# Optimization experiments

Hardware: AMD Instinct MI355X
Metric: run time of the kernel (lower is better)

## Reference

```python
import jax, jax.numpy as jnp
import numpy as np

N, E, G = 2000, 8000, 100          # nodes, edges, graphs
F_NODE, F_EDGE, H, FC = 22, 4, 128, 64
EPS = 1e-5                          # BatchNorm eps (eval mode, running stats)


def setup_inputs() -> dict:
    key = jax.random.key(0)
    ks = jax.random.split(key, 24)
    rn = lambda k, s, sc=0.1: jax.random.normal(k, s, jnp.float32) * sc
    inp = {}
    inp["x"] = jax.random.normal(ks[0], (N, F_NODE), jnp.float32)
    inp["edge_index"] = jax.random.randint(ks[1], (2, E), 0, N, jnp.int64)
    inp["edge_attr"] = jax.random.uniform(ks[2], (E, F_EDGE), jnp.float32)
    inp["batch"] = jnp.sort(jax.random.randint(ks[3], (N,), 0, G, jnp.int64))
    # edge networks (Linear + ReLU) producing per-edge weight matrices
    inp["We1"] = rn(ks[4], (F_EDGE, F_NODE * H)); inp["be1"] = jnp.zeros((F_NODE * H,), jnp.float32)
    inp["We2"] = rn(ks[5], (F_EDGE, H * H));      inp["be2"] = jnp.zeros((H * H,), jnp.float32)
    inp["We3"] = rn(ks[6], (F_EDGE, H * H));      inp["be3"] = jnp.zeros((H * H,), jnp.float32)
    # NNConv root weights + biases
    inp["Wr1"] = rn(ks[7], (F_NODE, H)); inp["br1"] = jnp.zeros((H,), jnp.float32)
    inp["Wr2"] = rn(ks[8], (H, H));      inp["br2"] = jnp.zeros((H,), jnp.float32)
    inp["Wr3"] = rn(ks[9], (H, H));      inp["br3"] = jnp.zeros((H,), jnp.float32)
    # BatchNorm (eval): gamma, beta, running_mean, running_var
    for i, k in zip((1, 2, 3), (ks[10], ks[11], ks[12])):
        inp[f"g{i}"] = 1.0 + rn(k, (H,), 0.05)
        inp[f"b{i}"] = jnp.zeros((H,), jnp.float32)
        inp[f"rm{i}"] = jnp.zeros((H,), jnp.float32)
        inp[f"rv{i}"] = jnp.ones((H,), jnp.float32)
    # head MLP
    inp["Wf1"] = rn(ks[13], (H, FC)); inp["bf1"] = jnp.zeros((FC,), jnp.float32)
    inp["Wf2"] = rn(ks[14], (FC, 1)); inp["bf2"] = jnp.zeros((1,), jnp.float32)
    return inp


def _nnconv(x, src, dst, edge_attr, We, be, Wr, br, din, dout):
    # per-edge weight matrix from edge features: [E, din, dout]
    w = jax.nn.relu(edge_attr @ We + be).reshape(-1, din, dout)
    msg = jnp.einsum('ei,eio->eo', x[src], w)          # gather + batched matvec
    agg = jax.ops.segment_sum(msg, dst, num_segments=N)  # scatter-add at targets
    return agg + x @ Wr + br                            # root transform + bias


def _bn(x, g, b, rm, rv):
    return (x - rm) * jax.lax.rsqrt(rv + EPS) * g + b


def reference(x, edge_index, edge_attr, batch,
              We1, be1, We2, be2, We3, be3,
              Wr1, br1, Wr2, br2, Wr3, br3,
              g1, b1, rm1, rv1, g2, b2, rm2, rv2, g3, b3, rm3, rv3,
              Wf1, bf1, Wf2, bf2):
    src, dst = edge_index[0], edge_index[1]
    h = jax.nn.relu(_bn(_nnconv(x, src, dst, edge_attr, We1, be1, Wr1, br1, F_NODE, H), g1, b1, rm1, rv1))
    h = jax.nn.relu(_bn(_nnconv(h, src, dst, edge_attr, We2, be2, Wr2, br2, H, H), g2, b2, rm2, rv2))
    h = jax.nn.relu(_bn(_nnconv(h, src, dst, edge_attr, We3, be3, Wr3, br3, H, H), g3, b3, rm3, rv3))
    # global mean pool over graphs
    sums = jax.ops.segment_sum(h, batch, num_segments=G)
    cnts = jax.ops.segment_sum(jnp.ones((N,), h.dtype), batch, num_segments=G)
    pooled = sums / jnp.maximum(cnts, 1.0)[:, None]
    # head MLP (dropout is identity at inference)
    out = jax.nn.relu(pooled @ Wf1 + bf1) @ Wf2 + bf2
    return out  # [G, 1]
```

## Files before the change

### kernel.cpp

```cpp
#include <hip/hip_runtime.h>
#include <hip/hip_bf16.h>
#include <math.h>

#define N_NODES 2000
#define N_EDGES 8000
#define N_GRAPH 100
#define F_NODE 22
#define F_EDGE 4
#define H 128
#define FC 64
#define EPSBN 1e-5f
#define EPB 16
#define EPT 8

#define C1  (F_NODE * H)
#define C1P (24 * H)
#define C2  (H * H)

__global__ __launch_bounds__(256) void precompute_kernel(
    const float* __restrict__ We1, const float* __restrict__ be1,
    const float* __restrict__ We2, const float* __restrict__ We3,
    const float* __restrict__ g1, const float* __restrict__ b1,
    const float* __restrict__ rm1, const float* __restrict__ rv1,
    const float* __restrict__ g2, const float* __restrict__ b2,
    const float* __restrict__ rm2, const float* __restrict__ rv2,
    const float* __restrict__ g3, const float* __restrict__ b3,
    const float* __restrict__ rm3, const float* __restrict__ rv3,
    float4* __restrict__ We1p, float* __restrict__ be1p,
    float4* __restrict__ We2p, float4* __restrict__ We3p,
    float* __restrict__ AB,
    float* __restrict__ sums, float* __restrict__ cnt)
{
    const int t = blockIdx.x * 256 + threadIdx.x;
    const int T1 = C1P, T2 = C1P + C2, T3 = C1P + 2 * C2, T4 = T3 + 3 * H;
    const int T5 = T4 + N_GRAPH * H + N_GRAPH;
    if (t < T1) {
        int j = t;
        if (j < C1) {
            We1p[j] = make_float4(We1[j], We1[C1 + j], We1[2 * C1 + j], We1[3 * C1 + j]);
            be1p[j] = be1[j];
        } else {
            We1p[j] = make_float4(0.f, 0.f, 0.f, 0.f);
            be1p[j] = 0.f;
        }
    } else if (t < T2) {
        int j = t - T1;
        We2p[j] = make_float4(We2[j], We2[C2 + j], We2[2 * C2 + j], We2[3 * C2 + j]);
    } else if (t < T3) {
        int j = t - T2;
        We3p[j] = make_float4(We3[j], We3[C2 + j], We3[2 * C2 + j], We3[3 * C2 + j]);
    } else if (t < T4) {
        int idx = t - T3;
        int l = idx / H, o = idx - l * H;
        const float *g, *b, *rm, *rv;
        if (l == 0) { g = g1; b = b1; rm = rm1; rv = rv1; }
        else if (l == 1) { g = g2; b = b2; rm = rm2; rv = rv2; }
        else { g = g3; b = b3; rm = rm3; rv = rv3; }
        float A = g[o] * rsqrtf(rv[o] + EPSBN);
        AB[l * 2 * H + o] = A;
        AB[l * 2 * H + H + o] = b[o] - rm[o] * A;
    } else if (t < T5) {
        int idx = t - T4;
        if (idx < N_GRAPH * H) sums[idx] = 0.f; else cnt[idx - N_GRAPH * H] = 0.f;
    }
}

template <int DIN, bool ACT>
__global__ __launch_bounds__(256) void root_kernel(
    const float* __restrict__ hin,
    const float* __restrict__ Wr,
    const float* __restrict__ br,
    const float* __restrict__ AB,
    float* __restrict__ outp)
{
    __shared__ float hs[2][DIN];
    const int n0 = blockIdx.x * 2;
    const int tid = threadIdx.x;
    for (int idx = tid; idx < 2 * DIN; idx += 256) {
        int nl = idx / DIN, i = idx - nl * DIN;
        float v = hin[(n0 + nl) * DIN + i];
        if (ACT) v = fmaxf(fmaf(v, AB[i], AB[H + i]), 0.f);
        hs[nl][i] = v;
    }
    __syncthreads();
    const int o = tid & 127;
    const int nl = tid >> 7;
    float acc = br[o];
#pragma unroll 4
    for (int i = 0; i < DIN; i++) acc = fmaf(hs[nl][i], Wr[i * H + o], acc);
    outp[(n0 + nl) * H + o] = acc;
}

template <int DIN, int ISPLIT, int UNR, bool ACT>
__global__ __launch_bounds__(256) void msg_kernel(
    const float* __restrict__ xin,
    const int* __restrict__ ei,
    const float* __restrict__ ea,
    const float4* __restrict__ Wp,
    const float* __restrict__ be,
    const float* __restrict__ AB,
    float* __restrict__ agg)
{
    constexpr int ILEN0 = DIN / ISPLIT;
    constexpr int ILEN = ((ILEN0 + UNR - 1) / UNR) * UNR;
    __shared__ float xs[EPB][ILEN];
    __shared__ float eas[EPB][4];
    __shared__ int dsts[EPB];

    const int nEB = N_EDGES / EPB;
    const int eb = blockIdx.x % nEB;
    const int I0 = (blockIdx.x / nEB) * ILEN0;
    const int e0 = eb * EPB;
    const int tid = threadIdx.x;

    if (tid < EPB * 4) {
        int e = tid >> 2, k = tid & 3;
        eas[e][k] = ea[(e0 + e) * 4 + k];
    }
    if (tid >= 64 && tid < 64 + EPB) {
        dsts[tid - 64] = ei[N_EDGES + e0 + (tid - 64)];
    }
    for (int idx = tid; idx < EPB * ILEN; idx += 256) {
        int e = idx / ILEN, ii = idx - e * ILEN;
        float v = 0.f;
        if (ii < ILEN0) {
            int s = ei[e0 + e];
            v = xin[s * DIN + I0 + ii];
            if (ACT) v = fmaxf(fmaf(v, AB[I0 + ii], AB[H + I0 + ii]), 0.f);
        }
        xs[e][ii] = v;
    }
    __syncthreads();

    const int o = tid & 127;
    const int eh = tid >> 7;

    float acc[EPT];
    float ear[EPT][4];
#pragma unroll
    for (int q = 0; q < EPT; q++) {
        acc[q] = 0.f;
#pragma unroll
        for (int k = 0; k < 4; k++) ear[q][k] = eas[eh * EPT + q][k];
    }

#pragma unroll 1
    for (int ii = 0; ii < ILEN; ii += UNR) {
        float4 w4[UNR];
        float bb[UNR];
#pragma unroll
        for (int u = 0; u < UNR; u++) {
            w4[u] = Wp[(I0 + ii + u) * H + o];
            bb[u] = be[(I0 + ii + u) * H + o];
        }
#pragma unroll
        for (int u = 0; u < UNR; u++) {
#pragma unroll
            for (int q = 0; q < EPT; q++) {
                float w = bb[u];
                w = fmaf(w4[u].x, ear[q][0], w);
                w = fmaf(w4[u].y, ear[q][1], w);
                w = fmaf(w4[u].z, ear[q][2], w);
                w = fmaf(w4[u].w, ear[q][3], w);
                w = fmaxf(w, 0.f);
                acc[q] = fmaf(xs[eh * EPT + q][ii + u], w, acc[q]);
            }
        }
    }

#pragma unroll
    for (int q = 0; q < EPT; q++) {
        atomicAdd(&agg[dsts[eh * EPT + q] * H + o], acc[q]);
    }
}

__global__ __launch_bounds__(128) void pool_kernel(
    const float* __restrict__ h, const int* __restrict__ batch,
    const float* __restrict__ AB,
    float* __restrict__ sums, float* __restrict__ cnt)
{
    const int n = blockIdx.x;
    const int o = threadIdx.x;
    const int gph = batch[n];
    float v = h[n * H + o];
    v = fmaxf(fmaf(v, AB[o], AB[H + o]), 0.f);
    atomicAdd(&sums[gph * H + o], v);
    if (o == 0) atomicAdd(&cnt[gph], 1.0f);
}

__global__ __launch_bounds__(64) void head_kernel(
    const float* __restrict__ sums, const float* __restrict__ cnt,
    const float* __restrict__ Wf1, const float* __restrict__ bf1,
    const float* __restrict__ Wf2, const float* __restrict__ bf2,
    float* __restrict__ out)
{
    const int gph = blockIdx.x;
    const int j = threadIdx.x;
    const float inv = 1.0f / fmaxf(cnt[gph], 1.0f);
    float f = bf1[j];
    for (int i = 0; i < H; i++) f = fmaf(sums[gph * H + i] * inv, Wf1[i * FC + j], f);
    f = fmaxf(f, 0.f);
    float p = f * Wf2[j];
#pragma unroll
    for (int off = 32; off; off >>= 1) p += __shfl_down(p, off);
    if (j == 0) out[gph] = p + bf2[0];
}

extern "C" void kernel_launch(void* const* d_in, const int* in_sizes, int n_in,
                              void* d_out, int out_size, void* d_ws, size_t ws_size,
                              hipStream_t stream) {
    const float* x   = (const float*)d_in[0];
    const int* ei    = (const int*)d_in[1];
    const float* ea  = (const float*)d_in[2];
    const int* batch = (const int*)d_in[3];
    const float* We1 = (const float*)d_in[4];
    const float* be1 = (const float*)d_in[5];
    const float* We2 = (const float*)d_in[6];
    const float* be2 = (const float*)d_in[7];
    const float* We3 = (const float*)d_in[8];
    const float* be3 = (const float*)d_in[9];
    const float* Wr1 = (const float*)d_in[10];
    const float* br1 = (const float*)d_in[11];
    const float* Wr2 = (const float*)d_in[12];
    const float* br2 = (const float*)d_in[13];
    const float* Wr3 = (const float*)d_in[14];
    const float* br3 = (const float*)d_in[15];
    const float* g1 = (const float*)d_in[16], *b1 = (const float*)d_in[17];
    const float* rm1 = (const float*)d_in[18], *rv1 = (const float*)d_in[19];
    const float* g2 = (const float*)d_in[20], *b2 = (const float*)d_in[21];
    const float* rm2 = (const float*)d_in[22], *rv2 = (const float*)d_in[23];
    const float* g3 = (const float*)d_in[24], *b3 = (const float*)d_in[25];
    const float* rm3 = (const float*)d_in[26], *rv3 = (const float*)d_in[27];
    const float* Wf1 = (const float*)d_in[28];
    const float* bf1 = (const float*)d_in[29];
    const float* Wf2 = (const float*)d_in[30];
    const float* bf2 = (const float*)d_in[31];

    float* out = (float*)d_out;

    float* ws = (float*)d_ws;
    float* h1   = ws;
    float* h2   = h1 + N_NODES * H;
    float* h3   = h2 + N_NODES * H;
    float* We1p = h3 + N_NODES * H;
    float* be1p = We1p + C1P * 4;
    float* We2p = be1p + C1P;
    float* We3p = We2p + C2 * 4;
    float* AB   = We3p + C2 * 4;
    float* sums = AB + 6 * H;
    float* cnt  = sums + N_GRAPH * H;

    const int PRE_T = C1P + 2 * C2 + 3 * H + N_GRAPH * H + N_GRAPH;
    precompute_kernel<<<(PRE_T + 255) / 256, 256, 0, stream>>>(
        We1, be1, We2, We3,
        g1, b1, rm1, rv1, g2, b2, rm2, rv2, g3, b3, rm3, rv3,
        (float4*)We1p, be1p, (float4*)We2p, (float4*)We3p, AB, sums, cnt);

    const int nEB = N_EDGES / EPB;

    root_kernel<F_NODE, false><<<N_NODES / 2, 256, 0, stream>>>(x, Wr1, br1, nullptr, h1);
    msg_kernel<F_NODE, 1, 4, false><<<nEB, 256, 0, stream>>>(x, ei, ea, (const float4*)We1p, be1p, nullptr, h1);

    root_kernel<H, true><<<N_NODES / 2, 256, 0, stream>>>(h1, Wr2, br2, AB + 0 * 2 * H, h2);
    msg_kernel<H, 2, 4, true><<<nEB * 2, 256, 0, stream>>>(h1, ei, ea, (const float4*)We2p, be2, AB + 0 * 2 * H, h2);

    root_kernel<H, true><<<N_NODES / 2, 256, 0, stream>>>(h2, Wr3, br3, AB + 1 * 2 * H, h3);
    msg_kernel<H, 2, 4, true><<<nEB * 2, 256, 0, stream>>>(h2, ei, ea, (const float4*)We3p, be3, AB + 1 * 2 * H, h3);

    pool_kernel<<<N_NODES, 128, 0, stream>>>(h3, batch, AB + 2 * 2 * H, sums, cnt);
    head_kernel<<<N_GRAPH, 64, 0, stream>>>(sums, cnt, Wf1, bf1, Wf2, bf2, out);
}
```

Baseline: 233.2 us.

## Vectorize bias and root loads, prefetch weights, fuse pool and head

```diff
diff --git a/kernel.cpp b/kernel.cpp
--- a/kernel.cpp
+++ b/kernel.cpp
@@ -19,38 +19,61 @@
 
 __global__ __launch_bounds__(256) void precompute_kernel(
     const float* __restrict__ We1, const float* __restrict__ be1,
-    const float* __restrict__ We2, const float* __restrict__ We3,
+    const float* __restrict__ We2, const float* __restrict__ be2,
+    const float* __restrict__ We3, const float* __restrict__ be3,
     const float* __restrict__ g1, const float* __restrict__ b1,
     const float* __restrict__ rm1, const float* __restrict__ rv1,
     const float* __restrict__ g2, const float* __restrict__ b2,
     const float* __restrict__ rm2, const float* __restrict__ rv2,
     const float* __restrict__ g3, const float* __restrict__ b3,
     const float* __restrict__ rm3, const float* __restrict__ rv3,
-    float4* __restrict__ We1p, float* __restrict__ be1p,
+    float4* __restrict__ We1p, float4* __restrict__ be1p4,
     float4* __restrict__ We2p, float4* __restrict__ We3p,
-    float* __restrict__ AB,
-    float* __restrict__ sums, float* __restrict__ cnt)
+    float4* __restrict__ be2p4, float4* __restrict__ be3p4,
+    float* __restrict__ AB)
 {
     const int t = blockIdx.x * 256 + threadIdx.x;
-    const int T1 = C1P, T2 = C1P + C2, T3 = C1P + 2 * C2, T4 = T3 + 3 * H;
-    const int T5 = T4 + N_GRAPH * H + N_GRAPH;
+    const int T1 = C1P;
+    const int T2 = T1 + 768;
+    const int T3 = T2 + C2;
+    const int T4 = T3 + C2;
+    const int T5 = T4 + 4096;
+    const int T6 = T5 + 4096;
+    const int T7 = T6 + 3 * H;
     if (t < T1) {
         int j = t;
-        if (j < C1) {
+        if (j < C1)
             We1p[j] = make_float4(We1[j], We1[C1 + j], We1[2 * C1 + j], We1[3 * C1 + j]);
-            be1p[j] = be1[j];
-        } else {
+        else
             We1p[j] = make_float4(0.f, 0.f, 0.f, 0.f);
-            be1p[j] = 0.f;
+    } else if (t < T2) {
+        int idx = t - T1;
+        int c = idx / H, o = idx - c * H;
+        float v[4];
+#pragma unroll
+        for (int u = 0; u < 4; u++) {
+            int r = 4 * c + u;
+            v[u] = (r < F_NODE) ? be1[r * H + o] : 0.f;
         }
-    } else if (t < T2) {
-        int j = t - T1;
-        We2p[j] = make_float4(We2[j], We2[C2 + j], We2[2 * C2 + j], We2[3 * C2 + j]);
+        be1p4[idx] = make_float4(v[0], v[1], v[2], v[3]);
     } else if (t < T3) {
         int j = t - T2;
+        We2p[j] = make_float4(We2[j], We2[C2 + j], We2[2 * C2 + j], We2[3 * C2 + j]);
+    } else if (t < T4) {
+        int j = t - T3;
         We3p[j] = make_float4(We3[j], We3[C2 + j], We3[2 * C2 + j], We3[3 * C2 + j]);
-    } else if (t < T4) {
-        int idx = t - T3;
+    } else if (t < T5) {
+        int idx = t - T4;
+        int c = idx / H, o = idx - c * H;
+        be2p4[idx] = make_float4(be2[(4 * c) * H + o], be2[(4 * c + 1) * H + o],
+                                 be2[(4 * c + 2) * H + o], be2[(4 * c + 3) * H + o]);
+    } else if (t < T6) {
+        int idx = t - T5;
+        int c = idx / H, o = idx - c * H;
+        be3p4[idx] = make_float4(be3[(4 * c) * H + o], be3[(4 * c + 1) * H + o],
+                                 be3[(4 * c + 2) * H + o], be3[(4 * c + 3) * H + o]);
+    } else if (t < T7) {
+        int idx = t - T6;
         int l = idx / H, o = idx - l * H;
         const float *g, *b, *rm, *rv;
         if (l == 0) { g = g1; b = b1; rm = rm1; rv = rv1; }
@@ -59,51 +82,77 @@
         float A = g[o] * rsqrtf(rv[o] + EPSBN);
         AB[l * 2 * H + o] = A;
         AB[l * 2 * H + H + o] = b[o] - rm[o] * A;
-    } else if (t < T5) {
-        int idx = t - T4;
-        if (idx < N_GRAPH * H) sums[idx] = 0.f; else cnt[idx - N_GRAPH * H] = 0.f;
     }
 }
 
 template <int DIN, bool ACT>
 __global__ __launch_bounds__(256) void root_kernel(
     const float* __restrict__ hin,
-    const float* __restrict__ Wr,
-    const float* __restrict__ br,
+    const float4* __restrict__ Wr4,
+    const float4* __restrict__ br4,
     const float* __restrict__ AB,
     float* __restrict__ outp)
 {
-    __shared__ float hs[2][DIN];
-    const int n0 = blockIdx.x * 2;
+    constexpr int NPB = 8;
+    __shared__ float hs[NPB][DIN];
+    const int n0 = blockIdx.x * NPB;
     const int tid = threadIdx.x;
-    for (int idx = tid; idx < 2 * DIN; idx += 256) {
+    for (int idx = tid; idx < NPB * DIN; idx += 256) {
         int nl = idx / DIN, i = idx - nl * DIN;
         float v = hin[(n0 + nl) * DIN + i];
         if (ACT) v = fmaxf(fmaf(v, AB[i], AB[H + i]), 0.f);
         hs[nl][i] = v;
     }
     __syncthreads();
-    const int o = tid & 127;
-    const int nl = tid >> 7;
-    float acc = br[o];
+    const int og = tid & 31;
+    const int nl = tid >> 5;
+    float4 acc = br4[og];
 #pragma unroll 4
-    for (int i = 0; i < DIN; i++) acc = fmaf(hs[nl][i], Wr[i * H + o], acc);
-    outp[(n0 + nl) * H + o] = acc;
-}
-
-template <int DIN, int ISPLIT, int UNR, bool ACT>
+    for (int i = 0; i < DIN; i++) {
+        float4 w = Wr4[i * (H / 4) + og];
+        float xv = hs[nl][i];
+        acc.x = fmaf(xv, w.x, acc.x);
+        acc.y = fmaf(xv, w.y, acc.y);
+        acc.z = fmaf(xv, w.z, acc.z);
+        acc.w = fmaf(xv, w.w, acc.w);
+    }
+    ((float4*)(outp + (n0 + nl) * H))[og] = acc;
+}
+
+#define COMP_CHUNK(WREG, BREG, BASE)                                           \
+  {                                                                            \
+    float bu_[4] = {BREG.x, BREG.y, BREG.z, BREG.w};                           \
+    _Pragma("unroll")                                                          \
+    for (int u = 0; u < 4; u++) {                                              \
+      float4 xa_ = *(const float4*)&xs[(BASE) + u][eh * EPT];                  \
+      float4 xb_ = *(const float4*)&xs[(BASE) + u][eh * EPT + 4];              \
+      float xq_[8] = {xa_.x, xa_.y, xa_.z, xa_.w, xb_.x, xb_.y, xb_.z, xb_.w}; \
+      float4 wv_ = WREG[u];                                                    \
+      _Pragma("unroll")                                                        \
+      for (int q = 0; q < 8; q++) {                                            \
+        float w_ = fmaf(wv_.x, ear[q][0], bu_[u]);                             \
+        w_ = fmaf(wv_.y, ear[q][1], w_);                                       \
+        w_ = fmaf(wv_.z, ear[q][2], w_);                                       \
+        w_ = fmaf(wv_.w, ear[q][3], w_);                                       \
+        w_ = fmaxf(w_, 0.f);                                                   \
+        acc[q] = fmaf(xq_[q], w_, acc[q]);                                     \
+      }                                                                        \
+    }                                                                          \
+  }
+
+template <int DIN, int ISPLIT, bool ACT>
 __global__ __launch_bounds__(256) void msg_kernel(
     const float* __restrict__ xin,
     const int* __restrict__ ei,
     const float* __restrict__ ea,
     const float4* __restrict__ Wp,
-    const float* __restrict__ be,
+    const float4* __restrict__ bp4,
     const float* __restrict__ AB,
     float* __restrict__ agg)
 {
     constexpr int ILEN0 = DIN / ISPLIT;
-    constexpr int ILEN = ((ILEN0 + UNR - 1) / UNR) * UNR;
-    __shared__ float xs[EPB][ILEN];
+    constexpr int ILEN = ((ILEN0 + 7) / 8) * 8;
+    __shared__ float xs[ILEN][EPB];
     __shared__ float eas[EPB][4];
     __shared__ int dsts[EPB];
 
@@ -121,22 +170,22 @@
         dsts[tid - 64] = ei[N_EDGES + e0 + (tid - 64)];
     }
     for (int idx = tid; idx < EPB * ILEN; idx += 256) {
-        int e = idx / ILEN, ii = idx - e * ILEN;
+        int i = idx >> 4, e = idx & 15;
         float v = 0.f;
-        if (ii < ILEN0) {
+        if (i < ILEN0) {
             int s = ei[e0 + e];
-            v = xin[s * DIN + I0 + ii];
-            if (ACT) v = fmaxf(fmaf(v, AB[I0 + ii], AB[H + I0 + ii]), 0.f);
+            v = xin[s * DIN + I0 + i];
+            if (ACT) v = fmaxf(fmaf(v, AB[I0 + i], AB[H + I0 + i]), 0.f);
         }
-        xs[e][ii] = v;
+        xs[i][e] = v;
     }
     __syncthreads();
 
     const int o = tid & 127;
     const int eh = tid >> 7;
 
+    float ear[EPT][4];
     float acc[EPT];
-    float ear[EPT][4];
 #pragma unroll
     for (int q = 0; q < EPT; q++) {
         acc[q] = 0.f;
@@ -144,28 +193,27 @@
         for (int k = 0; k < 4; k++) ear[q][k] = eas[eh * EPT + q][k];
     }
 
+    const float4* wp = Wp + I0 * H + o;
+    const float4* bp = bp4 + (I0 / 4) * H + o;
+
+    float4 wA[4], wB[4];
+    float4 bA, bB;
+#pragma unroll
+    for (int u = 0; u < 4; u++) wA[u] = wp[u * H];
+    bA = bp[0];
+
 #pragma unroll 1
-    for (int ii = 0; ii < ILEN; ii += UNR) {
-        float4 w4[UNR];
-        float bb[UNR];
-#pragma unroll
-        for (int u = 0; u < UNR; u++) {
-            w4[u] = Wp[(I0 + ii + u) * H + o];
-            bb[u] = be[(I0 + ii + u) * H + o];
+    for (int ii = 0; ii < ILEN; ii += 8) {
+#pragma unroll
+        for (int u = 0; u < 4; u++) wB[u] = wp[(ii + 4 + u) * H];
+        bB = bp[(ii / 4 + 1) * H];
+        COMP_CHUNK(wA, bA, ii)
+        if (ii + 8 < ILEN) {
+#pragma unroll
+            for (int u = 0; u < 4; u++) wA[u] = wp[(ii + 8 + u) * H];
+            bA = bp[(ii / 4 + 2) * H];
         }
-#pragma unroll
-        for (int u = 0; u < UNR; u++) {
-#pragma unroll
-            for (int q = 0; q < EPT; q++) {
-                float w = bb[u];
-                w = fmaf(w4[u].x, ear[q][0], w);
-                w = fmaf(w4[u].y, ear[q][1], w);
-                w = fmaf(w4[u].z, ear[q][2], w);
-                w = fmaf(w4[u].w, ear[q][3], w);
-                w = fmaxf(w, 0.f);
-                acc[q] = fmaf(xs[eh * EPT + q][ii + u], w, acc[q]);
-            }
-        }
+        COMP_CHUNK(wB, bB, ii + 4)
     }
 
 #pragma unroll
@@ -174,36 +222,43 @@
     }
 }
 
-__global__ __launch_bounds__(128) void pool_kernel(
+__global__ __launch_bounds__(128) void pool_head_kernel(
     const float* __restrict__ h, const int* __restrict__ batch,
     const float* __restrict__ AB,
-    float* __restrict__ sums, float* __restrict__ cnt)
-{
-    const int n = blockIdx.x;
-    const int o = threadIdx.x;
-    const int gph = batch[n];
-    float v = h[n * H + o];
-    v = fmaxf(fmaf(v, AB[o], AB[H + o]), 0.f);
-    atomicAdd(&sums[gph * H + o], v);
-    if (o == 0) atomicAdd(&cnt[gph], 1.0f);
-}
-
-__global__ __launch_bounds__(64) void head_kernel(
-    const float* __restrict__ sums, const float* __restrict__ cnt,
     const float* __restrict__ Wf1, const float* __restrict__ bf1,
     const float* __restrict__ Wf2, const float* __restrict__ bf2,
     float* __restrict__ out)
 {
-    const int gph = blockIdx.x;
-    const int j = threadIdx.x;
-    const float inv = 1.0f / fmaxf(cnt[gph], 1.0f);
-    float f = bf1[j];
-    for (int i = 0; i < H; i++) f = fmaf(sums[gph * H + i] * inv, Wf1[i * FC + j], f);
-    f = fmaxf(f, 0.f);
-    float p = f * Wf2[j];
-#pragma unroll
-    for (int off = 32; off; off >>= 1) p += __shfl_down(p, off);
-    if (j == 0) out[gph] = p + bf2[0];
+    __shared__ float pooled[H];
+    const int g = blockIdx.x;
+    const int t = threadIdx.x;
+
+    int a = 0, b = N_NODES;
+    while (a < b) { int m = (a + b) >> 1; if (batch[m] < g) a = m + 1; else b = m; }
+    const int lo = a;
+    b = N_NODES;
+    while (a < b) { int m = (a + b) >> 1; if (batch[m] < g + 1) a = m + 1; else b = m; }
+    const int hi = a;
+
+    float s = 0.f;
+    const float Ao = AB[t], Bo = AB[H + t];
+    for (int n = lo; n < hi; n++) {
+        float v = h[n * H + t];
+        s += fmaxf(fmaf(v, Ao, Bo), 0.f);
+    }
+    pooled[t] = (hi > lo) ? s / (float)(hi - lo) : 0.f;
+    __syncthreads();
+
+    if (t < FC) {
+        float f = bf1[t];
+#pragma unroll 4
+        for (int i = 0; i < H; i++) f = fmaf(pooled[i], Wf1[i * FC + t], f);
+        f = fmaxf(f, 0.f);
+        float p = f * Wf2[t];
+#pragma unroll
+        for (int off = 32; off; off >>= 1) p += __shfl_down(p, off);
+        if (t == 0) out[g] = p + bf2[0];
+    }
 }
 
 extern "C" void kernel_launch(void* const* d_in, const int* in_sizes, int n_in,
@@ -239,34 +294,41 @@
     float* out = (float*)d_out;
 
     float* ws = (float*)d_ws;
-    float* h1   = ws;
-    float* h2   = h1 + N_NODES * H;
-    float* h3   = h2 + N_NODES * H;
-    float* We1p = h3 + N_NODES * H;
-    float* be1p = We1p + C1P * 4;
-    float* We2p = be1p + C1P;
-    float* We3p = We2p + C2 * 4;
-    float* AB   = We3p + C2 * 4;
-    float* sums = AB + 6 * H;
-    float* cnt  = sums + N_GRAPH * H;
-
-    const int PRE_T = C1P + 2 * C2 + 3 * H + N_GRAPH * H + N_GRAPH;
+    float* h1    = ws;
+    float* h2    = h1 + N_NODES * H;
+    float* h3    = h2 + N_NODES * H;
+    float* We1p  = h3 + N_NODES * H;
+    float* We2p  = We1p + C1P * 4;
+    float* We3p  = We2p + C2 * 4;
+    float* be1p4 = We3p + C2 * 4;
+    float* be2p4 = be1p4 + 768 * 4;
+    float* be3p4 = be2p4 + 4096 * 4;
+    float* AB    = be3p4 + 4096 * 4;
+
+    const int PRE_T = C1P + 768 + 2 * C2 + 2 * 4096 + 3 * H;
     precompute_kernel<<<(PRE_T + 255) / 256, 256, 0, stream>>>(
-        We1, be1, We2, We3,
+        We1, be1, We2, be2, We3, be3,
         g1, b1, rm1, rv1, g2, b2, rm2, rv2, g3, b3, rm3, rv3,
-        (float4*)We1p, be1p, (float4*)We2p, (float4*)We3p, AB, sums, cnt);
+        (float4*)We1p, (float4*)be1p4, (float4*)We2p, (float4*)We3p,
+        (float4*)be2p4, (float4*)be3p4, AB);
 
     const int nEB = N_EDGES / EPB;
 
-    root_kernel<F_NODE, false><<<N_NODES / 2, 256, 0, stream>>>(x, Wr1, br1, nullptr, h1);
-    msg_kernel<F_NODE, 1, 4, false><<<nEB, 256, 0, stream>>>(x, ei, ea, (const float4*)We1p, be1p, nullptr, h1);
-
-    root_kernel<H, true><<<N_NODES / 2, 256, 0, stream>>>(h1, Wr2, br2, AB + 0 * 2 * H, h2);
-    msg_kernel<H, 2, 4, true><<<nEB * 2, 256, 0, stream>>>(h1, ei, ea, (const float4*)We2p, be2, AB + 0 * 2 * H, h2);
-
-    root_kernel<H, true><<<N_NODES / 2, 256, 0, stream>>>(h2, Wr3, br3, AB + 1 * 2 * H, h3);
-    msg_kernel<H, 2, 4, true><<<nEB * 2, 256, 0, stream>>>(h2, ei, ea, (const float4*)We3p, be3, AB + 1 * 2 * H, h3);
-
-    pool_kernel<<<N_NODES, 128, 0, stream>>>(h3, batch, AB + 2 * 2 * H, sums, cnt);
-    head_kernel<<<N_GRAPH, 64, 0, stream>>>(sums, cnt, Wf1, bf1, Wf2, bf2, out);
-}
+    root_kernel<F_NODE, false><<<N_NODES / 8, 256, 0, stream>>>(
+        x, (const float4*)Wr1, (const float4*)br1, nullptr, h1);
+    msg_kernel<F_NODE, 1, false><<<nEB, 256, 0, stream>>>(
+        x, ei, ea, (const float4*)We1p, (const float4*)be1p4, nullptr, h1);
+
+    root_kernel<H, true><<<N_NODES / 8, 256, 0, stream>>>(
+        h1, (const float4*)Wr2, (const float4*)br2, AB + 0 * 2 * H, h2);
+    msg_kernel<H, 2, true><<<nEB * 2, 256, 0, stream>>>(
+        h1, ei, ea, (const float4*)We2p, (const float4*)be2p4, AB + 0 * 2 * H, h2);
+
+    root_kernel<H, true><<<N_NODES / 8, 256, 0, stream>>>(
+        h2, (const float4*)Wr3, (const float4*)br3, AB + 1 * 2 * H, h3);
+    msg_kernel<H, 2, true><<<nEB * 2, 256, 0, stream>>>(
+        h2, ei, ea, (const float4*)We3p, (const float4*)be3p4, AB + 1 * 2 * H, h3);
+
+    pool_head_kernel<<<N_GRAPH, 128, 0, stream>>>(
+        h3, batch, AB + 2 * 2 * H, Wf1, bf1, Wf2, bf2, out);
+}
```

After: 219.0 us. -6.1%, faster.
